# Performance work log

Hardware: AMD Instinct MI355X
Metric: run time of the kernel (lower is better)

## Reference

```python
import jax, jax.numpy as jnp
import numpy as np

D_MODEL = 2048
NUM_HEADS = 16
HEAD_DIM = D_MODEL // NUM_HEADS
B, T = 4, 2048


def setup_inputs() -> dict:
    key = jax.random.key(0)
    ks = jax.random.split(key, 9)
    s = 1.0 / np.sqrt(D_MODEL)
    inp = {"x": jax.random.normal(ks[0], (B, T, D_MODEL), dtype=jnp.float32)}
    for i, name in enumerate(["q", "k", "v", "o"]):
        inp[f"W{name}"] = jax.random.uniform(ks[1 + 2 * i], (D_MODEL, D_MODEL), minval=-s, maxval=s, dtype=jnp.float32)
        inp[f"b{name}"] = jax.random.uniform(ks[2 + 2 * i], (D_MODEL,), minval=-s, maxval=s, dtype=jnp.float32)
    return inp


def reference(x, Wq, bq, Wk, bk, Wv, bv, Wo, bo):
    Bx, Tx, _ = x.shape
    H, Dh = NUM_HEADS, HEAD_DIM
    # torch Linear: y = x @ W.T + b
    q = (x @ Wq.T + bq).reshape(Bx, Tx, H, Dh).transpose(0, 2, 1, 3)  # [B,H,T,D]
    k = (x @ Wk.T + bk).reshape(Bx, Tx, H, Dh).transpose(0, 2, 1, 3)
    v = (x @ Wv.T + bv).reshape(Bx, Tx, H, Dh).transpose(0, 2, 1, 3)
    scale = 1.0 / np.sqrt(Dh).astype(np.float32)
    scores = jnp.einsum('bhqd,bhkd->bhqk', q, k) * scale  # [B,H,T,T] (no causal mask, as in source)
    attn = jax.nn.softmax(scores, axis=-1)
    out = jnp.einsum('bhqk,bhkd->bhqd', attn, v)  # [B,H,T,D]
    out = out.transpose(0, 2, 1, 3).reshape(Bx, Tx, H * Dh)
    return out @ Wo.T + bo
```

## Files before the change

kernel.cpp:

```cpp
#include <hip/hip_runtime.h>
#include <hip/hip_bf16.h>

typedef __bf16 bf16x8 __attribute__((ext_vector_type(8)));
typedef __bf16 bf16x4 __attribute__((ext_vector_type(4)));
typedef float floatx4 __attribute__((ext_vector_type(4)));

#define MFMA16(a, b, c) __builtin_amdgcn_mfma_f32_16x16x32_bf16((a), (b), (c), 0, 0, 0)

#define GLOAD16(g, l) __builtin_amdgcn_global_load_lds( \
    (const __attribute__((address_space(1))) unsigned int*)(g), \
    (__attribute__((address_space(3))) unsigned int*)(l), 16, 0, 0)

static constexpr int DM = 2048, NH = 16, HD = 128, BATCH = 4, SEQ = 2048;
static constexpr int MROWS = BATCH * SEQ;
static constexpr float SCALE = 0.08838834764831845f;
static constexpr float PMAX = 3.0f;

static constexpr size_t XE = (size_t)MROWS * DM;
static constexpr size_t WE = (size_t)DM * DM;

__global__ __launch_bounds__(256) void cvt_all(
    const float* __restrict__ x, const float* __restrict__ Wq,
    const float* __restrict__ Wk, const float* __restrict__ Wv,
    const float* __restrict__ Wo, __bf16* __restrict__ dst) {
  const size_t total = XE + 4 * WE;
  size_t stride = (size_t)gridDim.x * 256 * 8;
  for (size_t i = ((size_t)blockIdx.x * 256 + threadIdx.x) * 8; i < total; i += stride) {
    const float* src;
    size_t off;
    if (i < XE) { src = x; off = i; }
    else {
      size_t j = i - XE;
      int seg = (int)(j / WE);
      off = j - (size_t)seg * WE;
      src = seg == 0 ? Wq : (seg == 1 ? Wk : (seg == 2 ? Wv : Wo));
    }
    float4 a = *reinterpret_cast<const float4*>(src + off);
    float4 b = *reinterpret_cast<const float4*>(src + off + 4);
    bf16x8 r;
    r[0] = (__bf16)a.x; r[1] = (__bf16)a.y; r[2] = (__bf16)a.z; r[3] = (__bf16)a.w;
    r[4] = (__bf16)b.x; r[5] = (__bf16)b.y; r[6] = (__bf16)b.z; r[7] = (__bf16)b.w;
    *reinterpret_cast<bf16x8*>(dst + i) = r;
  }
}

__device__ __forceinline__ void gemm128_core(
    const __bf16* __restrict__ A, const __bf16* __restrict__ W,
    unsigned short* sA, unsigned short* sW,
    int tm, int tn, floatx4 (&acc)[4][4]) {
  const int tid = threadIdx.x;
  const int wave = tid >> 6, lane = tid & 63;
  const int q = lane >> 4, ml = lane & 15;
  const int waveM = (wave >> 1) * 64, waveN = (wave & 1) * 64;
  const int lrow = lane >> 3, cdst = lane & 7;
  const int csrc = cdst ^ (lrow & 7);

  for (int k0 = 0; k0 < DM; k0 += 64) {
    __syncthreads();
#pragma unroll
    for (int i = 0; i < 4; ++i) {
      int r0 = wave * 32 + i * 8;
      GLOAD16(A + (size_t)(tm + r0 + lrow) * DM + k0 + csrc * 8, &sA[r0 * 64]);
      GLOAD16(W + (size_t)(tn + r0 + lrow) * DM + k0 + csrc * 8, &sW[r0 * 64]);
    }
    __syncthreads();
#pragma unroll
    for (int s = 0; s < 2; ++s) {
      bf16x8 aF[4], bF[4];
#pragma unroll
      for (int t = 0; t < 4; ++t)
        aF[t] = *reinterpret_cast<const bf16x8*>(
            &sA[(waveM + t * 16 + ml) * 64 + (((s * 4 + q) ^ (ml & 7)) * 8)]);
#pragma unroll
      for (int t = 0; t < 4; ++t)
        bF[t] = *reinterpret_cast<const bf16x8*>(
            &sW[(waveN + t * 16 + ml) * 64 + (((s * 4 + q) ^ (ml & 7)) * 8)]);
#pragma unroll
      for (int rt = 0; rt < 4; ++rt)
#pragma unroll
        for (int ct = 0; ct < 4; ++ct)
          acc[rt][ct] = MFMA16(aF[rt], bF[ct], acc[rt][ct]);
    }
  }
}

__global__ __launch_bounds__(256) void qkv_gemm(
    const __bf16* __restrict__ X,
    const __bf16* __restrict__ Wq, const __bf16* __restrict__ Wk,
    const __bf16* __restrict__ Wv,
    const float* __restrict__ bq, const float* __restrict__ bk,
    const float* __restrict__ bv,
    __bf16* __restrict__ qh, __bf16* __restrict__ kh, __bf16* __restrict__ vt) {
  __shared__ unsigned short sA[128 * 64];
  __shared__ unsigned short sW[128 * 64];
  const int which = blockIdx.x >> 4;
  const int tn = (blockIdx.x & 15) * 128;
  const int tm = blockIdx.y * 128;
  const __bf16* W = which == 0 ? Wq : (which == 1 ? Wk : Wv);
  const float* bias = which == 0 ? bq : (which == 1 ? bk : bv);

  floatx4 acc[4][4] = {};
  gemm128_core(X, W, sA, sW, tm, tn, acc);

  const int tid = threadIdx.x, wave = tid >> 6, lane = tid & 63;
  const int q = lane >> 4, ml = lane & 15;
  const int waveM = (wave >> 1) * 64, waveN = (wave & 1) * 64;
#pragma unroll
  for (int ct = 0; ct < 4; ++ct) {
    int n = tn + waveN + ct * 16 + ml;
    float bv_ = bias[n];
    int h = n >> 7, d = n & 127;
#pragma unroll
    for (int rt = 0; rt < 4; ++rt) {
      int m0 = tm + waveM + rt * 16 + q * 4;
      int b = m0 >> 11, t = m0 & 2047;
      if (which < 2) {
        __bf16* dst = which == 0 ? qh : kh;
#pragma unroll
        for (int r = 0; r < 4; ++r)
          dst[((size_t)(b * 16 + h) * SEQ + t + r) * HD + d] = (__bf16)(acc[rt][ct][r] + bv_);
      } else {
        bf16x4 pk;
#pragma unroll
        for (int r = 0; r < 4; ++r) pk[r] = (__bf16)(acc[rt][ct][r] + bv_);
        *reinterpret_cast<bf16x4*>(vt + (size_t)((b * 16 + h) * 128 + d) * SEQ + t) = pk;
      }
    }
  }
}

__global__ __launch_bounds__(256) void proj_gemm(
    const __bf16* __restrict__ A, const __bf16* __restrict__ W,
    const float* __restrict__ bias, float* __restrict__ out) {
  __shared__ unsigned short sA[128 * 64];
  __shared__ unsigned short sW[128 * 64];
  const int tn = blockIdx.x * 128;
  const int tm = blockIdx.y * 128;

  floatx4 acc[4][4] = {};
  gemm128_core(A, W, sA, sW, tm, tn, acc);

  const int tid = threadIdx.x, wave = tid >> 6, lane = tid & 63;
  const int q = lane >> 4, ml = lane & 15;
  const int waveM = (wave >> 1) * 64, waveN = (wave & 1) * 64;
#pragma unroll
  for (int ct = 0; ct < 4; ++ct) {
    int n = tn + waveN + ct * 16 + ml;
    float bv_ = bias[n];
#pragma unroll
    for (int rt = 0; rt < 4; ++rt) {
      int m0 = tm + waveM + rt * 16 + q * 4;
#pragma unroll
      for (int r = 0; r < 4; ++r)
        out[(size_t)(m0 + r) * DM + n] = acc[rt][ct][r] + bv_;
    }
  }
}

__global__ __launch_bounds__(512) void mha_attn(
    const __bf16* __restrict__ Q, const __bf16* __restrict__ Kg,
    const __bf16* __restrict__ Vt, __bf16* __restrict__ O) {
  __shared__ unsigned short sK[64 * 128];
  __shared__ unsigned short sV[128 * 64];
  __shared__ unsigned short sP[128 * 72];

  const int tid = threadIdx.x;
  const int bh = blockIdx.x;
  const int t0 = blockIdx.y * 128;
  const int wave = tid >> 6, lane = tid & 63;
  const int q = lane >> 4, ml = lane & 15;
  const int wrow = wave * 16;

  bf16x8 qf[4];
  {
    const __bf16* qrow = Q + ((size_t)bh * SEQ + t0 + wrow + ml) * HD;
#pragma unroll
    for (int s = 0; s < 4; ++s)
      qf[s] = *reinterpret_cast<const bf16x8*>(qrow + s * 32 + q * 8);
  }

  floatx4 oacc[8] = {};
  float lsum[4] = {0.f, 0.f, 0.f, 0.f};

  const __bf16* kbase = Kg + (size_t)bh * SEQ * HD;
  const __bf16* vbase = Vt + (size_t)bh * HD * SEQ;
  const int lrow4 = lane >> 4, c16 = lane & 15;
  const int lrow8 = lane >> 3, c8 = lane & 7;

  for (int kt = 0; kt < SEQ / 64; ++kt) {
    const int key0 = kt * 64;
    __syncthreads();
#pragma unroll
    for (int i = 0; i < 2; ++i) {
      int kr0 = wave * 8 + i * 4;
      int kc = c16 ^ ((i * 4 + lrow4) & 7);
      GLOAD16(kbase + (size_t)(key0 + kr0 + lrow4) * HD + kc * 8, &sK[kr0 * 128]);
      int vr0 = wave * 16 + i * 8;
      int vc = c8 ^ (lrow8 & 7);
      GLOAD16(vbase + (size_t)(vr0 + lrow8) * SEQ + key0 + vc * 8, &sV[vr0 * 64]);
    }
    __syncthreads();

    floatx4 sacc[4] = {};
#pragma unroll
    for (int s = 0; s < 4; ++s) {
#pragma unroll
      for (int ct = 0; ct < 4; ++ct) {
        bf16x8 kf = *reinterpret_cast<const bf16x8*>(
            &sK[(ct * 16 + ml) * 128 + (((s * 4 + q) ^ (ml & 7)) * 8)]);
        sacc[ct] = MFMA16(qf[s], kf, sacc[ct]);
      }
    }

#pragma unroll
    for (int ct = 0; ct < 4; ++ct) {
#pragma unroll
      for (int r = 0; r < 4; ++r) {
        float p = __expf(fmaf(sacc[ct][r], SCALE, -PMAX));
        sacc[ct][r] = p;
        lsum[r] += p;
        __bf16 pb = (__bf16)p;
        sP[(wrow + q * 4 + r) * 72 + ct * 16 + ml] = __builtin_bit_cast(unsigned short, pb);
      }
    }

#pragma unroll
    for (int s = 0; s < 2; ++s) {
      bf16x8 pf = *reinterpret_cast<const bf16x8*>(&sP[(wrow + ml) * 72 + s * 32 + q * 8]);
#pragma unroll
      for (int ot = 0; ot < 8; ++ot) {
        bf16x8 vf = *reinterpret_cast<const bf16x8*>(
            &sV[(ot * 16 + ml) * 64 + (((s * 4 + q) ^ (ml & 7)) * 8)]);
        oacc[ot] = MFMA16(pf, vf, oacc[ot]);
      }
    }
  }

#pragma unroll
  for (int r = 0; r < 4; ++r) {
    float s = lsum[r];
    s += __shfl_xor(s, 1); s += __shfl_xor(s, 2);
    s += __shfl_xor(s, 4); s += __shfl_xor(s, 8);
    lsum[r] = 1.0f / s;
  }
  const int b = bh >> 4, h = bh & 15;
  __bf16* obase = O + ((size_t)b * SEQ + t0 + wrow) * DM + h * HD;
#pragma unroll
  for (int ot = 0; ot < 8; ++ot) {
    int d = ot * 16 + ml;
#pragma unroll
    for (int r = 0; r < 4; ++r)
      obase[(size_t)(q * 4 + r) * DM + d] = (__bf16)(oacc[ot][r] * lsum[r]);
  }
}

__device__ inline bf16x8 ld8s(const float* p) {
  float4 a = *reinterpret_cast<const float4*>(p);
  float4 b = *reinterpret_cast<const float4*>(p + 4);
  bf16x8 r;
  r[0] = (__bf16)a.x; r[1] = (__bf16)a.y; r[2] = (__bf16)a.z; r[3] = (__bf16)a.w;
  r[4] = (__bf16)b.x; r[5] = (__bf16)b.y; r[6] = (__bf16)b.z; r[7] = (__bf16)b.w;
  return r;
}
__device__ inline bf16x8 ld8s(const __bf16* p) {
  int4 v = *reinterpret_cast<const int4*>(p);
  return __builtin_bit_cast(bf16x8, v);
}

template <typename TA>
__global__ __launch_bounds__(256) void gemm_slow(
    const TA* __restrict__ A, const float* __restrict__ W,
    const float* __restrict__ bias, void* __restrict__ C, int mode, int out_f32) {
  __shared__ unsigned short sA[128 * 72];
  __shared__ unsigned short sW[128 * 72];
  const int tid = threadIdx.x;
  const int tn = blockIdx.x * 128, tm = blockIdx.y * 128;
  const int wave = tid >> 6, lane = tid & 63;
  const int q = lane >> 4, ml = lane & 15;
  const int waveM = (wave >> 1) * 64, waveN = (wave & 1) * 64;
  const int srow = tid >> 3, sc8 = tid & 7;
  floatx4 acc[4][4] = {};
  for (int k0 = 0; k0 < DM; k0 += 64) {
    bf16x8 va[4], vb[4];
#pragma unroll
    for (int i = 0; i < 4; ++i) {
      int row = srow + 32 * i;
      va[i] = ld8s(A + (size_t)(tm + row) * DM + k0 + sc8 * 8);
      vb[i] = ld8s(W + (size_t)(tn + row) * DM + k0 + sc8 * 8);
    }
    __syncthreads();
#pragma unroll
    for (int i = 0; i < 4; ++i) {
      int row = srow + 32 * i;
      *reinterpret_cast<int4*>(&sA[row * 72 + sc8 * 8]) = __builtin_bit_cast(int4, va[i]);
      *reinterpret_cast<int4*>(&sW[row * 72 + sc8 * 8]) = __builtin_bit_cast(int4, vb[i]);
    }
    __syncthreads();
#pragma unroll
    for (int s = 0; s < 2; ++s) {
      bf16x8 aF[4], bF[4];
#pragma unroll
      for (int t = 0; t < 4; ++t)
        aF[t] = *reinterpret_cast<const bf16x8*>(&sA[(waveM + t * 16 + ml) * 72 + s * 32 + q * 8]);
#pragma unroll
      for (int t = 0; t < 4; ++t)
        bF[t] = *reinterpret_cast<const bf16x8*>(&sW[(waveN + t * 16 + ml) * 72 + s * 32 + q * 8]);
#pragma unroll
      for (int rt = 0; rt < 4; ++rt)
#pragma unroll
        for (int ct = 0; ct < 4; ++ct)
          acc[rt][ct] = MFMA16(aF[rt], bF[ct], acc[rt][ct]);
    }
  }
#pragma unroll
  for (int ct = 0; ct < 4; ++ct) {
    int n = tn + waveN + ct * 16 + ml;
    float bv = bias[n];
    int h = n >> 7, d = n & 127;
#pragma unroll
    for (int rt = 0; rt < 4; ++rt) {
      int m0 = tm + waveM + rt * 16 + q * 4;
      int b = m0 >> 11, t = m0 & 2047;
      if (mode == 0) {
        if (out_f32) {
#pragma unroll
          for (int r = 0; r < 4; ++r)
            ((float*)C)[(size_t)(m0 + r) * DM + n] = acc[rt][ct][r] + bv;
        } else {
#pragma unroll
          for (int r = 0; r < 4; ++r)
            ((__bf16*)C)[(size_t)(m0 + r) * DM + n] = (__bf16)(acc[rt][ct][r] + bv);
        }
      } else if (mode == 1) {
        bf16x4 pk;
#pragma unroll
        for (int r = 0; r < 4; ++r) pk[r] = (__bf16)(acc[rt][ct][r] + bv);
        *reinterpret_cast<bf16x4*>((__bf16*)C + (size_t)((b * 16 + h) * 128 + d) * SEQ + t) = pk;
      } else {
#pragma unroll
        for (int r = 0; r < 4; ++r)
          ((__bf16*)C)[((size_t)(b * 16 + h) * SEQ + t + r) * HD + d] =
              (__bf16)(acc[rt][ct][r] + bv);
      }
    }
  }
}

extern "C" void kernel_launch(void* const* d_in, const int* in_sizes, int n_in,
                              void* d_out, int out_size, void* d_ws, size_t ws_size,
                              hipStream_t stream) {
  const float* x  = (const float*)d_in[0];
  const float* Wq = (const float*)d_in[1]; const float* bq = (const float*)d_in[2];
  const float* Wk = (const float*)d_in[3]; const float* bk = (const float*)d_in[4];
  const float* Wv = (const float*)d_in[5]; const float* bv = (const float*)d_in[6];
  const float* Wo = (const float*)d_in[7]; const float* bo = (const float*)d_in[8];

  const size_t needA = 64 + 2 * (4 * XE + 4 * WE);
  dim3 gq(48, 64), gp(16, 64), ga(BATCH * NH, SEQ / 128);

  if (ws_size >= needA + 256) {
    __bf16* xc  = (__bf16*)((char*)d_ws + 64);
    __bf16* Wqc = xc + XE;
    __bf16* Wkc = Wqc + WE;
    __bf16* Wvc = Wkc + WE;
    __bf16* Woc = Wvc + WE;
    __bf16* qh  = Woc + WE;
    __bf16* kh  = qh + XE;
    __bf16* vt  = kh + XE;
    __bf16* aw  = xc;

    cvt_all<<<4096, 256, 0, stream>>>(x, Wq, Wk, Wv, Wo, xc);
    qkv_gemm<<<gq, 256, 0, stream>>>(xc, Wqc, Wkc, Wvc, bq, bk, bv, qh, kh, vt);
    mha_attn<<<ga, 512, 0, stream>>>(qh, kh, vt, aw);
    proj_gemm<<<gp, 256, 0, stream>>>(aw, Woc, bo, (float*)d_out);
  } else {
    __bf16* qh = (__bf16*)((char*)d_ws + 64);
    __bf16* kh = qh + XE;
    __bf16* vt = kh + XE;
    __bf16* aw = vt + XE;
    gemm_slow<float><<<gp, 256, 0, stream>>>(x, Wq, bq, qh, 2, 0);
    gemm_slow<float><<<gp, 256, 0, stream>>>(x, Wk, bk, kh, 2, 0);
    gemm_slow<float><<<gp, 256, 0, stream>>>(x, Wv, bv, vt, 1, 0);
    mha_attn<<<ga, 512, 0, stream>>>(qh, kh, vt, aw);
    gemm_slow<__bf16><<<gp, 256, 0, stream>>>(aw, Wo, bo, d_out, 0, 1);
  }
}
```

Before: 731.0 us.

## Replace 128x128 GEMM with 4-stage pipelined 256x256 tile GEMM

Both the QKV and output projection GEMMs move from a 128x128 tile with a single-buffered 64-wide K loop to a 256x256 tile with 512 threads. The new loop uses a 4-deep ring of 32-wide K slabs loaded with global_load_lds, and waits with vmcnt instead of full syncthreads. It also raises wave priority around the MFMA block. The goal is to hide global-to-LDS latency and raise arithmetic intensity per LDS byte, at the cost of more registers (8x4 accumulators), more LDS, and fewer blocks per grid, which could hurt occupancy and wave balance.

```diff
diff --git a/kernel.cpp b/kernel.cpp
--- a/kernel.cpp
+++ b/kernel.cpp
@@ -44,115 +44,136 @@
   }
 }
 
-__device__ __forceinline__ void gemm128_core(
+__device__ __forceinline__ void gemm256_core(
     const __bf16* __restrict__ A, const __bf16* __restrict__ W,
-    unsigned short* sA, unsigned short* sW,
-    int tm, int tn, floatx4 (&acc)[4][4]) {
+    unsigned short* sA, unsigned short* sB,
+    int tm, int tn, floatx4 (&acc)[8][4]) {
   const int tid = threadIdx.x;
   const int wave = tid >> 6, lane = tid & 63;
   const int q = lane >> 4, ml = lane & 15;
-  const int waveM = (wave >> 1) * 64, waveN = (wave & 1) * 64;
-  const int lrow = lane >> 3, cdst = lane & 7;
-  const int csrc = cdst ^ (lrow & 7);
-
-  for (int k0 = 0; k0 < DM; k0 += 64) {
-    __syncthreads();
-#pragma unroll
-    for (int i = 0; i < 4; ++i) {
-      int r0 = wave * 32 + i * 8;
-      GLOAD16(A + (size_t)(tm + r0 + lrow) * DM + k0 + csrc * 8, &sA[r0 * 64]);
-      GLOAD16(W + (size_t)(tn + r0 + lrow) * DM + k0 + csrc * 8, &sW[r0 * 64]);
-    }
-    __syncthreads();
-#pragma unroll
-    for (int s = 0; s < 2; ++s) {
-      bf16x8 aF[4], bF[4];
-#pragma unroll
-      for (int t = 0; t < 4; ++t)
-        aF[t] = *reinterpret_cast<const bf16x8*>(
-            &sA[(waveM + t * 16 + ml) * 64 + (((s * 4 + q) ^ (ml & 7)) * 8)]);
-#pragma unroll
-      for (int t = 0; t < 4; ++t)
-        bF[t] = *reinterpret_cast<const bf16x8*>(
-            &sW[(waveN + t * 16 + ml) * 64 + (((s * 4 + q) ^ (ml & 7)) * 8)]);
-#pragma unroll
-      for (int rt = 0; rt < 4; ++rt)
-#pragma unroll
-        for (int ct = 0; ct < 4; ++ct)
-          acc[rt][ct] = MFMA16(aF[rt], bF[ct], acc[rt][ct]);
-    }
-  }
-}
-
-__global__ __launch_bounds__(256) void qkv_gemm(
+  const int wm = wave >> 2, wn = wave & 3;
+
+  const int csrc = (tid & 3) ^ ((tid >> 3) & 3);
+  const __bf16* gA = A + (size_t)(tm + (tid >> 2)) * DM + csrc * 8;
+  const __bf16* gB = W + (size_t)(tn + (tid >> 2)) * DM + csrc * 8;
+  const size_t rstep = (size_t)128 * DM;
+  const int ldsW = wave * 512;
+
+  const int fsw = (q ^ ((ml >> 1) & 3)) * 8;
+  const int aOff = (wm * 128 + ml) * 32 + fsw;
+  const int bOff = (wn * 64 + ml) * 32 + fsw;
+
+#define STAGE256(s_) do { \
+    const int _r = ((s_) & 3) * 8192;   \
+    const int _k = (s_) * 32;           \
+    GLOAD16(gA + _k,         sA + _r + ldsW); \
+    GLOAD16(gA + _k + rstep, sA + _r + 4096 + ldsW); \
+    GLOAD16(gB + _k,         sB + _r + ldsW); \
+    GLOAD16(gB + _k + rstep, sB + _r + 4096 + ldsW); \
+  } while (0)
+
+  STAGE256(0); STAGE256(1); STAGE256(2);
+  asm volatile("s_waitcnt vmcnt(8)" ::: "memory");
+  __builtin_amdgcn_s_barrier();
+
+#pragma unroll 4
+  for (int p = 0; p < 64; ++p) {
+    const int regO = (p & 3) * 8192;
+    bf16x8 aF[8], bF[4];
+#pragma unroll
+    for (int t = 0; t < 8; ++t)
+      aF[t] = *reinterpret_cast<const bf16x8*>(sA + regO + aOff + t * 512);
+#pragma unroll
+    for (int t = 0; t < 4; ++t)
+      bF[t] = *reinterpret_cast<const bf16x8*>(sB + regO + bOff + t * 512);
+
+    STAGE256((p + 3) & 63);
+    asm volatile("s_waitcnt vmcnt(8)" ::: "memory");
+    __builtin_amdgcn_s_barrier();
+
+    __builtin_amdgcn_s_setprio(1);
+#pragma unroll
+    for (int mt = 0; mt < 8; ++mt)
+#pragma unroll
+      for (int ct = 0; ct < 4; ++ct)
+        acc[mt][ct] = MFMA16(aF[mt], bF[ct], acc[mt][ct]);
+    __builtin_amdgcn_s_setprio(0);
+    __builtin_amdgcn_s_barrier();
+    asm volatile("" ::: "memory");
+  }
+#undef STAGE256
+}
+
+__global__ __launch_bounds__(512, 2) void qkv_gemm256(
     const __bf16* __restrict__ X,
     const __bf16* __restrict__ Wq, const __bf16* __restrict__ Wk,
     const __bf16* __restrict__ Wv,
     const float* __restrict__ bq, const float* __restrict__ bk,
     const float* __restrict__ bv,
     __bf16* __restrict__ qh, __bf16* __restrict__ kh, __bf16* __restrict__ vt) {
-  __shared__ unsigned short sA[128 * 64];
-  __shared__ unsigned short sW[128 * 64];
-  const int which = blockIdx.x >> 4;
-  const int tn = (blockIdx.x & 15) * 128;
-  const int tm = blockIdx.y * 128;
+  __shared__ unsigned short sA[4 * 256 * 32];
+  __shared__ unsigned short sB[4 * 256 * 32];
+  const int bx = blockIdx.x;
+  const int which = bx >> 3;
+  const int tn = (bx & 7) * 256;
+  const int tm = blockIdx.y * 256;
   const __bf16* W = which == 0 ? Wq : (which == 1 ? Wk : Wv);
   const float* bias = which == 0 ? bq : (which == 1 ? bk : bv);
 
-  floatx4 acc[4][4] = {};
-  gemm128_core(X, W, sA, sW, tm, tn, acc);
+  floatx4 acc[8][4] = {};
+  gemm256_core(X, W, sA, sB, tm, tn, acc);
 
   const int tid = threadIdx.x, wave = tid >> 6, lane = tid & 63;
   const int q = lane >> 4, ml = lane & 15;
-  const int waveM = (wave >> 1) * 64, waveN = (wave & 1) * 64;
+  const int wm = wave >> 2, wn = wave & 3;
 #pragma unroll
   for (int ct = 0; ct < 4; ++ct) {
-    int n = tn + waveN + ct * 16 + ml;
+    int n = tn + wn * 64 + ct * 16 + ml;
     float bv_ = bias[n];
     int h = n >> 7, d = n & 127;
 #pragma unroll
-    for (int rt = 0; rt < 4; ++rt) {
-      int m0 = tm + waveM + rt * 16 + q * 4;
+    for (int mt = 0; mt < 8; ++mt) {
+      int m0 = tm + wm * 128 + mt * 16 + q * 4;
       int b = m0 >> 11, t = m0 & 2047;
       if (which < 2) {
         __bf16* dst = which == 0 ? qh : kh;
 #pragma unroll
         for (int r = 0; r < 4; ++r)
-          dst[((size_t)(b * 16 + h) * SEQ + t + r) * HD + d] = (__bf16)(acc[rt][ct][r] + bv_);
+          dst[((size_t)(b * 16 + h) * SEQ + t + r) * HD + d] = (__bf16)(acc[mt][ct][r] + bv_);
       } else {
         bf16x4 pk;
 #pragma unroll
-        for (int r = 0; r < 4; ++r) pk[r] = (__bf16)(acc[rt][ct][r] + bv_);
+        for (int r = 0; r < 4; ++r) pk[r] = (__bf16)(acc[mt][ct][r] + bv_);
         *reinterpret_cast<bf16x4*>(vt + (size_t)((b * 16 + h) * 128 + d) * SEQ + t) = pk;
       }
     }
   }
 }
 
-__global__ __launch_bounds__(256) void proj_gemm(
+__global__ __launch_bounds__(512, 2) void proj_gemm256(
     const __bf16* __restrict__ A, const __bf16* __restrict__ W,
     const float* __restrict__ bias, float* __restrict__ out) {
-  __shared__ unsigned short sA[128 * 64];
-  __shared__ unsigned short sW[128 * 64];
-  const int tn = blockIdx.x * 128;
-  const int tm = blockIdx.y * 128;
-
-  floatx4 acc[4][4] = {};
-  gemm128_core(A, W, sA, sW, tm, tn, acc);
+  __shared__ unsigned short sA[4 * 256 * 32];
+  __shared__ unsigned short sB[4 * 256 * 32];
+  const int tn = blockIdx.x * 256;
+  const int tm = blockIdx.y * 256;
+
+  floatx4 acc[8][4] = {};
+  gemm256_core(A, W, sA, sB, tm, tn, acc);
 
   const int tid = threadIdx.x, wave = tid >> 6, lane = tid & 63;
   const int q = lane >> 4, ml = lane & 15;
-  const int waveM = (wave >> 1) * 64, waveN = (wave & 1) * 64;
+  const int wm = wave >> 2, wn = wave & 3;
 #pragma unroll
   for (int ct = 0; ct < 4; ++ct) {
-    int n = tn + waveN + ct * 16 + ml;
+    int n = tn + wn * 64 + ct * 16 + ml;
     float bv_ = bias[n];
 #pragma unroll
-    for (int rt = 0; rt < 4; ++rt) {
-      int m0 = tm + waveM + rt * 16 + q * 4;
+    for (int mt = 0; mt < 8; ++mt) {
+      int m0 = tm + wm * 128 + mt * 16 + q * 4;
 #pragma unroll
       for (int r = 0; r < 4; ++r)
-        out[(size_t)(m0 + r) * DM + n] = acc[rt][ct][r] + bv_;
+        out[(size_t)(m0 + r) * DM + n] = acc[mt][ct][r] + bv_;
     }
   }
 }
@@ -356,7 +377,7 @@
   const float* Wo = (const float*)d_in[7]; const float* bo = (const float*)d_in[8];
 
   const size_t needA = 64 + 2 * (4 * XE + 4 * WE);
-  dim3 gq(48, 64), gp(16, 64), ga(BATCH * NH, SEQ / 128);
+  dim3 gq(24, 32), gp(8, 32), gs(16, 64), ga(BATCH * NH, SEQ / 128);
 
   if (ws_size >= needA + 256) {
     __bf16* xc  = (__bf16*)((char*)d_ws + 64);
@@ -370,18 +391,18 @@
     __bf16* aw  = xc;
 
     cvt_all<<<4096, 256, 0, stream>>>(x, Wq, Wk, Wv, Wo, xc);
-    qkv_gemm<<<gq, 256, 0, stream>>>(xc, Wqc, Wkc, Wvc, bq, bk, bv, qh, kh, vt);
+    qkv_gemm256<<<gq, 512, 0, stream>>>(xc, Wqc, Wkc, Wvc, bq, bk, bv, qh, kh, vt);
     mha_attn<<<ga, 512, 0, stream>>>(qh, kh, vt, aw);
-    proj_gemm<<<gp, 256, 0, stream>>>(aw, Woc, bo, (float*)d_out);
+    proj_gemm256<<<gp, 512, 0, stream>>>(aw, Woc, bo, (float*)d_out);
   } else {
     __bf16* qh = (__bf16*)((char*)d_ws + 64);
     __bf16* kh = qh + XE;
     __bf16* vt = kh + XE;
     __bf16* aw = vt + XE;
-    gemm_slow<float><<<gp, 256, 0, stream>>>(x, Wq, bq, qh, 2, 0);
-    gemm_slow<float><<<gp, 256, 0, stream>>>(x, Wk, bk, kh, 2, 0);
-    gemm_slow<float><<<gp, 256, 0, stream>>>(x, Wv, bv, vt, 1, 0);
+    gemm_slow<float><<<gs, 256, 0, stream>>>(x, Wq, bq, qh, 2, 0);
+    gemm_slow<float><<<gs, 256, 0, stream>>>(x, Wk, bk, kh, 2, 0);
+    gemm_slow<float><<<gs, 256, 0, stream>>>(x, Wv, bv, vt, 1, 0);
     mha_attn<<<ga, 512, 0, stream>>>(qh, kh, vt, aw);
-    gemm_slow<__bf16><<<gp, 256, 0, stream>>>(aw, Wo, bo, d_out, 0, 1);
-  }
-}
+    gemm_slow<__bf16><<<gs, 256, 0, stream>>>(aw, Wo, bo, d_out, 0, 1);
+  }
+}
```

Measured after the change: 656.1 us. 1.11x faster.
